# Performance work log

Measured on AMD Instinct MI355X. Metric: run time of the kernel, lower is better.

The kernel has to match this reference:

```python
import jax, jax.numpy as jnp
import numpy as np

DIM = 768
NUM_BLOCKS = 4
BLOCK = DIM // NUM_BLOCKS
SCALE = 0.02


def setup_inputs() -> dict:
    key = jax.random.key(0)
    ks = jax.random.split(key, 7)
    x = jax.random.normal(ks[0], (8, 64, 64, DIM), dtype=jnp.float32)
    w1 = SCALE * jax.random.normal(ks[1], (2, NUM_BLOCKS, BLOCK, BLOCK), dtype=jnp.float32)
    b1 = SCALE * jax.random.normal(ks[2], (2, NUM_BLOCKS, BLOCK), dtype=jnp.float32)
    w2 = SCALE * jax.random.normal(ks[3], (2, NUM_BLOCKS, BLOCK, BLOCK), dtype=jnp.float32)
    b2 = SCALE * jax.random.normal(ks[4], (2, NUM_BLOCKS, BLOCK), dtype=jnp.float32)
    # nn.Linear(dim, dim) weight/bias (kaiming-uniform-ish init; exact init irrelevant for correctness)
    lim = 1.0 / np.sqrt(DIM)
    bias_w = jax.random.uniform(ks[5], (DIM, DIM), minval=-lim, maxval=lim, dtype=jnp.float32)
    bias_b = jax.random.uniform(ks[6], (DIM,), minval=-lim, maxval=lim, dtype=jnp.float32)
    return {"x": x, "w1": w1, "b1": b1, "w2": w2, "b2": b2, "bias_w": bias_w, "bias_b": bias_b}


def _block_mul(t, w):
    # t: (..., nb, bs), w: (nb, bs, bs) -> (..., nb, bs)
    return jnp.einsum('...bd,bdk->...bk', t, w)


def reference(x, w1, b1, w2, b2, bias_w, bias_b):
    B, H, W, C = x.shape
    nb = w1.shape[1]
    bs = C // nb
    bias = x @ bias_w.T + bias_b  # nn.Linear on original x
    xb = x.reshape(B, H, W, nb, bs)
    xf = jnp.fft.rfftn(xb, axes=(1, 2), norm='ortho')  # (B, H, W//2+1, nb, bs) complex
    xr, xi = xf.real, xf.imag
    # layer 1: complex block matmul + bias + relu (relu applied per real/imag part as in source)
    r1 = jax.nn.relu(_block_mul(xr, w1[0]) - _block_mul(xi, w1[1]) + b1[0])
    i1 = jax.nn.relu(_block_mul(xr, w1[1]) + _block_mul(xi, w1[0]) + b1[1])
    # layer 2: NOTE the original torch code reassigns x_real first and then uses the NEW
    # x_real when computing x_imag — we faithfully reproduce that.
    r2 = _block_mul(r1, w2[0]) - _block_mul(i1, w2[1]) + b2[0]
    i2 = _block_mul(r2, w2[1]) + _block_mul(i1, w2[0]) + b2[1]
    xc = jax.lax.complex(r2, i2)
    out = jnp.fft.irfftn(xc, s=(H, W), axes=(1, 2), norm='ortho')
    out = out.reshape(B, H, W, C)
    return out + bias
```

## Files before the change

kernel.cpp:

```cpp
#include <hip/hip_runtime.h>

#define DIM 768
#define NBLK 4
#define BS 192
#define BATCH 8
#define HH 64
#define WW 64
#define KH 33
#define NPTS (BATCH*HH*KH)
#define TWOPI_OVER_64 0.0981747704246810387f
#define LROW 200
#define WSZ (NBLK*BS*BS)

typedef __attribute__((ext_vector_type(8))) short short8;
typedef __attribute__((ext_vector_type(4))) short short4v;
typedef __attribute__((ext_vector_type(4))) float floatx4;
typedef __attribute__((ext_vector_type(4))) unsigned int uint4v;

static __device__ __forceinline__ short f2bs(float f) {
  union { float f; unsigned int i; } v; v.f = f;
  unsigned int x = v.i;
  return (short)((x + 0x7fffu + ((x >> 16) & 1u)) >> 16);
}
static __device__ __forceinline__ float bs2f(short s) {
  union { unsigned int i; float f; } v; v.i = ((unsigned int)(unsigned short)s) << 16; return v.f;
}

#define GLD16(gp, lp) \
  __builtin_amdgcn_global_load_lds( \
      (const __attribute__((address_space(1))) unsigned int*)(gp), \
      (__attribute__((address_space(3))) unsigned int*)(lp), 16, 0, 0)

__global__ __launch_bounds__(256) void k_convx(
    const float* __restrict__ X, short* __restrict__ Xb)
{
  const int i = blockIdx.x * 256 + threadIdx.x;
  const float4* X4 = (const float4*)X;
  #pragma unroll
  for (int it = 0; it < 12; ++it) {
    const int idx = i + it * (2048 * 256);
    const float4 v = X4[idx];
    short4v p = { f2bs(v.x), f2bs(v.y), f2bs(v.z), f2bs(v.w) };
    *(short4v*)&Xb[(size_t)idx * 4] = p;
  }
}

__global__ __launch_bounds__(256) void k_convw(
    const float* __restrict__ W, short* __restrict__ Wb)
{
  const int idx = blockIdx.x * 256 + threadIdx.x;
  const float4 v = ((const float4*)W)[idx];
  short4v p = { f2bs(v.x), f2bs(v.y), f2bs(v.z), f2bs(v.w) };
  *(short4v*)&Wb[(size_t)idx * 4] = p;
}

__global__ __launch_bounds__(256) void k_bias_gemm3(
    const short* __restrict__ Xb, const short* __restrict__ Wb,
    const float* __restrict__ bb, short* __restrict__ Bias)
{
  __shared__ short As[128 * 32];
  __shared__ short Bs[128 * 32];
  const int t = threadIdx.x;
  const int wave = t >> 6, lane = t & 63;
  const int qm = lane & 15, quad = lane >> 4;
  const int wr = (wave >> 1) * 64;
  const int wc = (wave & 1) * 64;
  const int m0 = blockIdx.x * 128, n0 = blockIdx.y * 128;

  floatx4 acc[4][4];
  const floatx4 zero = {0.f, 0.f, 0.f, 0.f};
  #pragma unroll
  for (int ms = 0; ms < 4; ++ms)
    #pragma unroll
    for (int ns = 0; ns < 4; ++ns) acc[ms][ns] = zero;

  const int r0 = t >> 2,        kq0 = (t & 3) * 8;
  const int r1 = (t + 256) >> 2;
  const short* gA0 = &Xb[(size_t)(m0 + r0) * DIM + kq0];
  const short* gA1 = &Xb[(size_t)(m0 + r1) * DIM + kq0];
  const short* gB0 = &Wb[(size_t)(n0 + r0) * DIM + kq0];
  const short* gB1 = &Wb[(size_t)(n0 + r1) * DIM + kq0];
  short* lA0 = &As[wave * 512];
  short* lA1 = &As[wave * 512 + 2048];
  short* lB0 = &Bs[wave * 512];
  short* lB1 = &Bs[wave * 512 + 2048];

  #pragma unroll 1
  for (int k0 = 0; k0 < DIM; k0 += 32) {
    __syncthreads();
    GLD16(gA0 + k0, lA0);
    GLD16(gA1 + k0, lA1);
    GLD16(gB0 + k0, lB0);
    GLD16(gB1 + k0, lB1);
    __syncthreads();

    short8 af[4], bf[4];
    #pragma unroll
    for (int ms = 0; ms < 4; ++ms)
      af[ms] = *(const short8*)&As[(wr + ms*16 + qm) * 32 + quad * 8];
    #pragma unroll
    for (int ns = 0; ns < 4; ++ns)
      bf[ns] = *(const short8*)&Bs[(wc + ns*16 + qm) * 32 + quad * 8];
    #pragma unroll
    for (int ms = 0; ms < 4; ++ms)
      #pragma unroll
      for (int ns = 0; ns < 4; ++ns)
        acc[ms][ns] = __builtin_amdgcn_mfma_f32_16x16x32_bf16(af[ms], bf[ns], acc[ms][ns], 0, 0, 0);
  }

  #pragma unroll
  for (int ns = 0; ns < 4; ++ns) {
    const int col = n0 + wc + ns*16 + qm;
    const float bias = bb[col];
    #pragma unroll
    for (int ms = 0; ms < 4; ++ms)
      #pragma unroll
      for (int r = 0; r < 4; ++r) {
        const int row = m0 + wr + ms*16 + quad*4 + r;
        Bias[(size_t)row * DIM + col] = f2bs(acc[ms][ns][r] + bias);
      }
  }
}

__global__ __launch_bounds__(256) void k_rfft_w_mfma(
    const short* __restrict__ Xb,
    short* __restrict__ Sr, short* __restrict__ Si)
{
  __shared__ short Lx[96 * 72];
  const int t = threadIdx.x;
  const int wave = t >> 6, lane = t & 63;
  const int qm = lane & 15, quad = lane >> 4;
  const int bh = blockIdx.x;
  const int c0 = blockIdx.y * 96;
  const size_t xbase = (size_t)bh * (WW*DIM);
  const size_t obase = (size_t)bh * (KH*DIM);

  #pragma unroll
  for (int it = 0; it < 3; ++it) {
    const int i = t + it * 256;
    const int hd = i & 31;
    const int c4 = i >> 5;
    const size_t g0 = xbase + (size_t)(2*hd) * DIM + c0 + c4 * 4;
    const short4v ra = *(const short4v*)&Xb[g0];
    const short4v rb = *(const short4v*)&Xb[g0 + DIM];
    #pragma unroll
    for (int e = 0; e < 4; ++e) {
      const int d = (c4*4 + e) * 36 + hd;
      ((unsigned*)Lx)[d] = (unsigned)(unsigned short)ra[e] |
                           ((unsigned)(unsigned short)rb[e] << 16);
    }
  }

  short8 Trh[2], Trl[2], Tih[2], Til[2];
  const int krow = wave * 16 + qm;
  #pragma unroll
  for (int kk = 0; kk < 2; ++kk) {
    #pragma unroll
    for (int j = 0; j < 8; ++j) {
      const int w = quad * 8 + j + kk * 32;
      const int ph = (krow * w) & 63;
      float s, c;
      sincosf((float)ph * TWOPI_OVER_64, &s, &c);
      const float tr = c, ti = -s;
      const short trh = f2bs(tr);
      const short tih = f2bs(ti);
      Trh[kk][j] = trh;  Trl[kk][j] = f2bs(tr - bs2f(trh));
      Tih[kk][j] = tih;  Til[kk][j] = f2bs(ti - bs2f(tih));
    }
  }
  __syncthreads();

  if (wave < 3) {
    const floatx4 zero = {0.f, 0.f, 0.f, 0.f};
    #pragma unroll 1
    for (int ct = 0; ct < 6; ++ct) {
      floatx4 Cr = zero, Ci = zero;
      #pragma unroll
      for (int kk = 0; kk < 2; ++kk) {
        const int a = (ct*16 + qm) * 72 + kk*32 + quad*8;
        const short8 xv = *(const short8*)&Lx[a];
        Cr = __builtin_amdgcn_mfma_f32_16x16x32_bf16(Trh[kk], xv, Cr, 0,0,0);
        Cr = __builtin_amdgcn_mfma_f32_16x16x32_bf16(Trl[kk], xv, Cr, 0,0,0);
        Ci = __builtin_amdgcn_mfma_f32_16x16x32_bf16(Tih[kk], xv, Ci, 0,0,0);
        Ci = __builtin_amdgcn_mfma_f32_16x16x32_bf16(Til[kk], xv, Ci, 0,0,0);
      }
      #pragma unroll
      for (int r = 0; r < 4; ++r) {
        const int ko = wave*16 + quad*4 + r;
        if (ko < KH) {
          const size_t o = obase + (size_t)ko * DIM + c0 + ct*16 + qm;
          Sr[o] = f2bs(Cr[r]);
          Si[o] = f2bs(Ci[r]);
        }
      }
    }
  }
}

__global__ __launch_bounds__(256) void k_prep_w(
    const float* __restrict__ w1, const float* __restrict__ w2,
    short* __restrict__ Wout)
{
  const int arr = blockIdx.y;
  const int i = blockIdx.x * 256 + threadIdx.x;
  const int nb = i / (BS*BS);
  const int rem = i % (BS*BS);
  const int n = rem / BS;
  const int d = rem % BS;
  const float* src = (arr < 2) ? w1 : w2;
  const int j = arr & 1;
  const float s = (arr == 3) ? -1.f : 1.f;
  const float v = s * src[((size_t)(j*NBLK + nb) * BS + d) * BS + n];
  Wout[(size_t)arr * WSZ + i] = f2bs(v);
}

__global__ __launch_bounds__(256) void k_prep_w2(
    const float* __restrict__ w2, const float* __restrict__ b2,
    short* __restrict__ Wout, float* __restrict__ b2x)
{
  const int i = blockIdx.x * 256 + threadIdx.x;
  const int n = i % BS;
  const int d = (i / BS) % BS;
  const int nb = i / (BS*BS);
  const float* R = w2 + (size_t)nb * BS * BS;
  const float* I = w2 + ((size_t)NBLK + nb) * BS * BS;
  const float* br = b2 + nb * BS;
  float ri = 0.f, ii = 0.f, bx = 0.f;
  #pragma unroll 4
  for (int m = 0; m < BS; ++m) {
    const float win = I[m*BS + n];
    ri += R[d*BS + m] * win;
    ii += I[d*BS + m] * win;
    bx += br[m] * win;
  }
  const size_t o = ((size_t)nb * BS + n) * BS + d;
  Wout[(size_t)4 * WSZ + o] = f2bs(ri);
  Wout[(size_t)5 * WSZ + o] = f2bs(R[d*BS + n] - ii);
  if (d == 0) b2x[nb * BS + n] = b2[(NBLK + nb) * BS + n] + bx;
}

__global__ __launch_bounds__(256) void k_fmix(
    short* __restrict__ Sr, short* __restrict__ Si,
    const short* __restrict__ WT,
    const float* __restrict__ b1, const float* __restrict__ b2,
    const float* __restrict__ b2x)
{
  __shared__ short U[2 * 64 * LROW];
  short* Ldr = U;
  short* Ldi = U + 192 * 64;
  short* Amr = U;
  short* Ami = U + 64 * LROW;

  const int t = threadIdx.x;
  const int wave = t >> 6, lane = t & 63;
  const int qm = lane & 15, quad = lane >> 4;
  const int bk = blockIdx.x;
  const int b = bk / KH, k = bk % KH;
  const int nb = blockIdx.y;
  const int c0 = nb * BS;
  const size_t hstride = (size_t)KH * DIM;
  const size_t base = ((size_t)b * HH * KH + k) * DIM;

  short8 Ch[2], Cl[2], Sh[2], Sl[2], SNh[2], SNl[2];
  const int hp = wave * 16 + qm;
  #pragma unroll
  for (int kk = 0; kk < 2; ++kk)
    #pragma unroll
    for (int j = 0; j < 8; ++j) {
      const int h = quad*8 + j + kk*32;
      const int ph = (hp * h) & 63;
      float s, c;
      sincosf((float)ph * TWOPI_OVER_64, &s, &c);
      const short ch = f2bs(c), sh = f2bs(s);
      Ch[kk][j] = ch;  Cl[kk][j] = f2bs(c - bs2f(ch));
      Sh[kk][j] = sh;  Sl[kk][j] = f2bs(s - bs2f(sh));
      SNh[kk][j] = (short)(sh ^ (short)0x8000);
      SNl[kk][j] = (short)(Sl[kk][j] ^ (short)0x8000);
    }

  #pragma unroll
  for (int it = 0; it < 6; ++it) {
    const int i = t + it * 256;
    const int hd = i & 31;
    const int c4 = i >> 5;
    const size_t g0 = base + (size_t)(2*hd) * hstride + c0 + c4 * 4;
    const short4v ra = *(const short4v*)&Sr[g0];
    const short4v rb = *(const short4v*)&Sr[g0 + hstride];
    const short4v ia = *(const short4v*)&Si[g0];
    const short4v ib = *(const short4v*)&Si[g0 + hstride];
    #pragma unroll
    for (int e = 0; e < 4; ++e) {
      const int c = c4*4 + e;
      const int d = c * 32 + (hd ^ ((c & 7) << 2));
      ((unsigned*)Ldr)[d] = (unsigned)(unsigned short)ra[e] |
                            ((unsigned)(unsigned short)rb[e] << 16);
      ((unsigned*)Ldi)[d] = (unsigned)(unsigned short)ia[e] |
                            ((unsigned)(unsigned short)ib[e] << 16);
    }
  }
  __syncthreads();

  const floatx4 zero = {0.f, 0.f, 0.f, 0.f};
  floatx4 Fr[12], Fi[12];
  #pragma unroll
  for (int ct = 0; ct < 12; ++ct) { Fr[ct] = zero; Fi[ct] = zero; }
  #pragma unroll
  for (int ct = 0; ct < 12; ++ct)
    #pragma unroll
    for (int kk = 0; kk < 2; ++kk) {
      const int a = (ct*16 + qm) * 64 + ((kk*32 + quad*8) ^ ((qm & 7) << 3));
      const short8 sr = *(const short8*)&Ldr[a];
      const short8 si = *(const short8*)&Ldi[a];
      Fr[ct] = __builtin_amdgcn_mfma_f32_16x16x32_bf16(Ch[kk],  sr, Fr[ct], 0,0,0);
      Fr[ct] = __builtin_amdgcn_mfma_f32_16x16x32_bf16(Cl[kk],  sr, Fr[ct], 0,0,0);
      Fr[ct] = __builtin_amdgcn_mfma_f32_16x16x32_bf16(Sh[kk],  si, Fr[ct], 0,0,0);
      Fr[ct] = __builtin_amdgcn_mfma_f32_16x16x32_bf16(Sl[kk],  si, Fr[ct], 0,0,0);
      Fi[ct] = __builtin_amdgcn_mfma_f32_16x16x32_bf16(SNh[kk], sr, Fi[ct], 0,0,0);
      Fi[ct] = __builtin_amdgcn_mfma_f32_16x16x32_bf16(SNl[kk], sr, Fi[ct], 0,0,0);
      Fi[ct] = __builtin_amdgcn_mfma_f32_16x16x32_bf16(Ch[kk],  si, Fi[ct], 0,0,0);
      Fi[ct] = __builtin_amdgcn_mfma_f32_16x16x32_bf16(Cl[kk],  si, Fi[ct], 0,0,0);
    }
  __syncthreads();

  #pragma unroll
  for (int ct = 0; ct < 12; ++ct)
    #pragma unroll
    for (int r = 0; r < 4; ++r) {
      const int row = wave*16 + quad*4 + r;
      const int c = ct*16 + qm;
      Amr[row * LROW + c] = f2bs(Fr[ct][r] * 0.015625f);
      Ami[row * LROW + c] = f2bs(Fi[ct][r] * 0.015625f);
    }
  __syncthreads();

  const short* W1R  = WT;
  const short* W1I  = WT + 1 * (size_t)WSZ;
  const short* W2R  = WT + 2 * (size_t)WSZ;
  const short* W2IN = WT + 3 * (size_t)WSZ;
  const short* W2RI = WT + 4 * (size_t)WSZ;
  const short* W2X  = WT + 5 * (size_t)WSZ;

  int nl[3];
  size_t wb[3];
  #pragma unroll
  for (int nt = 0; nt < 3; ++nt) {
    nl[nt] = wave * 48 + nt * 16 + qm;
    wb[nt] = (size_t)(c0 + nl[nt]) * BS + quad * 8;
  }

  floatx4 aR[4][3], aI[4][3];
  #pragma unroll
  for (int ms = 0; ms < 4; ++ms)
    #pragma unroll
    for (int nt = 0; nt < 3; ++nt) { aR[ms][nt] = zero; aI[ms][nt] = zero; }

  #pragma unroll 1
  for (int k0 = 0; k0 < BS; k0 += 32) {
    short8 xr[4], xi[4];
    #pragma unroll
    for (int ms = 0; ms < 4; ++ms) {
      const int a = (ms*16 + qm) * LROW + k0 + quad * 8;
      xr[ms] = *(const short8*)&Amr[a];
      xi[ms] = *(const short8*)&Ami[a];
    }
    #pragma unroll
    for (int nt = 0; nt < 3; ++nt) {
      const short8 br = *(const short8*)&W1R[wb[nt] + k0];
      const short8 bi = *(const short8*)&W1I[wb[nt] + k0];
      short8 bin;
      *(uint4v*)&bin = *(const uint4v*)&bi ^ 0x80008000u;
      #pragma unroll
      for (int ms = 0; ms < 4; ++ms) {
        aR[ms][nt] = __builtin_amdgcn_mfma_f32_16x16x32_bf16(xr[ms], br,  aR[ms][nt], 0,0,0);
        aR[ms][nt] = __builtin_amdgcn_mfma_f32_16x16x32_bf16(xi[ms], bin, aR[ms][nt], 0,0,0);
        aI[ms][nt] = __builtin_amdgcn_mfma_f32_16x16x32_bf16(xr[ms], bi,  aI[ms][nt], 0,0,0);
        aI[ms][nt] = __builtin_amdgcn_mfma_f32_16x16x32_bf16(xi[ms], br,  aI[ms][nt], 0,0,0);
      }
    }
  }
  __syncthreads();
  #pragma unroll
  for (int nt = 0; nt < 3; ++nt) {
    const float b1r = b1[nb * BS + nl[nt]];
    const float b1i = b1[(NBLK + nb) * BS + nl[nt]];
    #pragma unroll
    for (int ms = 0; ms < 4; ++ms)
      #pragma unroll
      for (int r = 0; r < 4; ++r) {
        const int row = ms*16 + quad*4 + r;
        Amr[row * LROW + nl[nt]] = f2bs(fmaxf(aR[ms][nt][r] + b1r, 0.f));
        Ami[row * LROW + nl[nt]] = f2bs(fmaxf(aI[ms][nt][r] + b1i, 0.f));
      }
  }
  __syncthreads();

  floatx4 c2r[4][3], c2i[4][3];
  #pragma unroll
  for (int ms = 0; ms < 4; ++ms)
    #pragma unroll
    for (int nt = 0; nt < 3; ++nt) { c2r[ms][nt] = zero; c2i[ms][nt] = zero; }

  #pragma unroll 1
  for (int k0 = 0; k0 < BS; k0 += 32) {
    short8 r1[4], i1[4];
    #pragma unroll
    for (int ms = 0; ms < 4; ++ms) {
      const int a = (ms*16 + qm) * LROW + k0 + quad * 8;
      r1[ms] = *(const short8*)&Amr[a];
      i1[ms] = *(const short8*)&Ami[a];
    }
    #pragma unroll
    for (int nt = 0; nt < 3; ++nt) {
      const short8 w_r  = *(const short8*)&W2R [wb[nt] + k0];
      const short8 w_in = *(const short8*)&W2IN[wb[nt] + k0];
      const short8 w_ri = *(const short8*)&W2RI[wb[nt] + k0];
      const short8 w_x  = *(const short8*)&W2X [wb[nt] + k0];
      #pragma unroll
      for (int ms = 0; ms < 4; ++ms) {
        c2r[ms][nt] = __builtin_amdgcn_mfma_f32_16x16x32_bf16(r1[ms], w_r,  c2r[ms][nt], 0,0,0);
        c2r[ms][nt] = __builtin_amdgcn_mfma_f32_16x16x32_bf16(i1[ms], w_in, c2r[ms][nt], 0,0,0);
        c2i[ms][nt] = __builtin_amdgcn_mfma_f32_16x16x32_bf16(r1[ms], w_ri, c2i[ms][nt], 0,0,0);
        c2i[ms][nt] = __builtin_amdgcn_mfma_f32_16x16x32_bf16(i1[ms], w_x,  c2i[ms][nt], 0,0,0);
      }
    }
  }
  __syncthreads();

  #pragma unroll
  for (int nt = 0; nt < 3; ++nt) {
    const float b2r = b2 [nb * BS + nl[nt]];
    const float bxi = b2x[nb * BS + nl[nt]];
    const int c = nl[nt];
    #pragma unroll
    for (int ms = 0; ms < 4; ++ms)
      #pragma unroll
      for (int r = 0; r < 4; ++r) {
        const int row = ms*16 + quad*4 + r;
        const int d = c * 64 + (row ^ ((c & 7) << 3));
        Ldr[d] = f2bs(c2r[ms][nt][r] + b2r);
        Ldi[d] = f2bs(c2i[ms][nt][r] + bxi);
      }
  }
  __syncthreads();

  #pragma unroll 1
  for (int ct = 0; ct < 12; ++ct) {
    floatx4 Cr = zero, Ci = zero;
    #pragma unroll
    for (int kk = 0; kk < 2; ++kk) {
      const int a = (ct*16 + qm) * 64 + ((kk*32 + quad*8) ^ ((qm & 7) << 3));
      const short8 gr = *(const short8*)&Ldr[a];
      const short8 gi = *(const short8*)&Ldi[a];
      Cr = __builtin_amdgcn_mfma_f32_16x16x32_bf16(Ch[kk],  gr, Cr, 0,0,0);
      Cr = __builtin_amdgcn_mfma_f32_16x16x32_bf16(Cl[kk],  gr, Cr, 0,0,0);
      Cr = __builtin_amdgcn_mfma_f32_16x16x32_bf16(SNh[kk], gi, Cr, 0,0,0);
      Cr = __builtin_amdgcn_mfma_f32_16x16x32_bf16(SNl[kk], gi, Cr, 0,0,0);
      Ci = __builtin_amdgcn_mfma_f32_16x16x32_bf16(Sh[kk],  gr, Ci, 0,0,0);
      Ci = __builtin_amdgcn_mfma_f32_16x16x32_bf16(Sl[kk],  gr, Ci, 0,0,0);
      Ci = __builtin_amdgcn_mfma_f32_16x16x32_bf16(Ch[kk],  gi, Ci, 0,0,0);
      Ci = __builtin_amdgcn_mfma_f32_16x16x32_bf16(Cl[kk],  gi, Ci, 0,0,0);
    }
    #pragma unroll
    for (int r = 0; r < 4; ++r) {
      const int hpo = wave*16 + quad*4 + r;
      const size_t o = base + (size_t)hpo * hstride + c0 + ct*16 + qm;
      Sr[o] = f2bs(Cr[r]);
      Si[o] = f2bs(Ci[r]);
    }
  }
}

__global__ __launch_bounds__(256) void k_irfft_w_mfma(
    const short* __restrict__ Sr, const short* __restrict__ Si,
    const short* __restrict__ Bias, float* __restrict__ out)
{
  __shared__ short Lr[96 * 72];
  __shared__ short Li[96 * 72];
  const int t = threadIdx.x;
  const int wave = t >> 6, lane = t & 63;
  const int qm = lane & 15, quad = lane >> 4;
  const int bh = blockIdx.x;
  const int c0 = blockIdx.y * 96;
  const size_t gbase = (size_t)bh * (KH*DIM);
  const size_t obase = (size_t)bh * (WW*DIM);

  #pragma unroll
  for (int it = 0; it < 3; ++it) {
    const int i = t + it * 256;
    const int hd = i & 31;
    const int c4 = i >> 5;
    const int ka = 2*hd, kb = 2*hd + 1;
    short4v ra = {0,0,0,0}, rb = ra, ia = ra, ib = ra;
    if (ka < KH) {
      const size_t g0 = gbase + (size_t)ka * DIM + c0 + c4 * 4;
      ra = *(const short4v*)&Sr[g0];
      ia = *(const short4v*)&Si[g0];
    }
    if (kb < KH) {
      const size_t g1 = gbase + (size_t)kb * DIM + c0 + c4 * 4;
      rb = *(const short4v*)&Sr[g1];
      ib = *(const short4v*)&Si[g1];
    }
    #pragma unroll
    for (int e = 0; e < 4; ++e) {
      const int d = (c4*4 + e) * 36 + hd;
      ((unsigned*)Lr)[d] = (unsigned)(unsigned short)ra[e] |
                           ((unsigned)(unsigned short)rb[e] << 16);
      ((unsigned*)Li)[d] = (unsigned)(unsigned short)ia[e] |
                           ((unsigned)(unsigned short)ib[e] << 16);
    }
  }

  short8 Arh[2], Arl[2], Aih[2], Ail[2];
  const int wrow = wave * 16 + qm;
  #pragma unroll
  for (int kk = 0; kk < 2; ++kk) {
    #pragma unroll
    for (int j = 0; j < 8; ++j) {
      const int k = quad * 8 + j + kk * 32;
      float ar = 0.f, ai = 0.f;
      if (k < KH) {
        const int ph = (wrow * k) & 63;
        float s, c;
        sincosf((float)ph * TWOPI_OVER_64, &s, &c);
        const float ck = (k == 0 || k == 32) ? (1.0f/64.0f) : (2.0f/64.0f);
        ar = ck * c;
        ai = -ck * s;
      }
      const short arh = f2bs(ar);
      const short aih = f2bs(ai);
      Arh[kk][j] = arh;  Arl[kk][j] = f2bs(ar - bs2f(arh));
      Aih[kk][j] = aih;  Ail[kk][j] = f2bs(ai - bs2f(aih));
    }
  }
  __syncthreads();

  const floatx4 zero = {0.f, 0.f, 0.f, 0.f};
  #pragma unroll 1
  for (int ct = 0; ct < 6; ++ct) {
    floatx4 C = zero;
    #pragma unroll
    for (int kk = 0; kk < 2; ++kk) {
      const int a = (ct*16 + qm) * 72 + kk*32 + quad*8;
      const short8 gr = *(const short8*)&Lr[a];
      const short8 gi = *(const short8*)&Li[a];
      C = __builtin_amdgcn_mfma_f32_16x16x32_bf16(Arh[kk], gr, C, 0,0,0);
      C = __builtin_amdgcn_mfma_f32_16x16x32_bf16(Arl[kk], gr, C, 0,0,0);
      C = __builtin_amdgcn_mfma_f32_16x16x32_bf16(Aih[kk], gi, C, 0,0,0);
      C = __builtin_amdgcn_mfma_f32_16x16x32_bf16(Ail[kk], gi, C, 0,0,0);
    }
    #pragma unroll
    for (int r = 0; r < 4; ++r) {
      const int w = wave*16 + quad*4 + r;
      const size_t o = obase + (size_t)w * DIM + c0 + ct*16 + qm;
      out[o] = C[r] + bs2f(Bias[o]);
    }
  }
}

extern "C" void kernel_launch(void* const* d_in, const int* in_sizes, int n_in,
                              void* d_out, int out_size, void* d_ws, size_t ws_size,
                              hipStream_t stream) {
  const float* x  = (const float*)d_in[0];
  const float* w1 = (const float*)d_in[1];
  const float* b1 = (const float*)d_in[2];
  const float* w2 = (const float*)d_in[3];
  const float* b2 = (const float*)d_in[4];
  const float* bw = (const float*)d_in[5];
  const float* bb = (const float*)d_in[6];
  float* out = (float*)d_out;

  short* Sr = (short*)d_ws;
  short* Si = Sr + (size_t)NPTS * DIM;
  short* WT = Si + (size_t)NPTS * DIM;
  short* Xb = WT + (size_t)6 * WSZ;
  short* Wb = Xb + (size_t)BATCH * HH * WW * DIM;
  short* Bias = Wb + (size_t)DIM * DIM;
  float* b2x = (float*)(Bias + (size_t)BATCH * HH * WW * DIM);

  k_convx<<<2048, 256, 0, stream>>>(x, Xb);
  k_convw<<<(DIM*DIM/4)/256, 256, 0, stream>>>(bw, Wb);
  k_prep_w<<<dim3(WSZ/256, 4), 256, 0, stream>>>(w1, w2, WT);
  k_prep_w2<<<dim3(WSZ/256), 256, 0, stream>>>(w2, b2, WT, b2x);
  k_bias_gemm3<<<dim3(32768/128, DIM/128), 256, 0, stream>>>(Xb, Wb, bb, Bias);
  k_rfft_w_mfma<<<dim3(BATCH*HH, DIM/96), 256, 0, stream>>>(Xb, Sr, Si);
  k_fmix<<<dim3(BATCH*KH, NBLK), 256, 0, stream>>>(Sr, Si, WT, b1, b2, b2x);
  k_irfft_w_mfma<<<dim3(BATCH*HH, DIM/96), 256, 0, stream>>>(Sr, Si, Bias, out);
}
```

Before: 493.5 us.

## Issue global loads early to overlap with twiddle setup and prefetch weights

In the rfft, irfft and fmix kernels, global loads are hoisted into registers before the sincos twiddle generation, so memory latency overlaps with trig computation; the LDS stores happen afterwards. fmix switches to 16-byte loads and a padded LDS layout (stride 72) instead of the XOR swizzle. It also software-prefetches the next W1 k-slice during layer-1 MFMAs and batches the W2 loads ahead of their MFMA loop. Register pressure and LDS footprint grow, which may reduce occupancy, and the padded layout may change bank-conflict behaviour.

```diff
diff --git a/kernel.cpp b/kernel.cpp
--- a/kernel.cpp
+++ b/kernel.cpp
@@ -135,20 +135,15 @@
   const size_t xbase = (size_t)bh * (WW*DIM);
   const size_t obase = (size_t)bh * (KH*DIM);
 
+  const int hd = t & 31;
+  const int c4b = t >> 5;
+  short4v ra[3], rb[3];
   #pragma unroll
   for (int it = 0; it < 3; ++it) {
-    const int i = t + it * 256;
-    const int hd = i & 31;
-    const int c4 = i >> 5;
+    const int c4 = c4b + it * 8;
     const size_t g0 = xbase + (size_t)(2*hd) * DIM + c0 + c4 * 4;
-    const short4v ra = *(const short4v*)&Xb[g0];
-    const short4v rb = *(const short4v*)&Xb[g0 + DIM];
-    #pragma unroll
-    for (int e = 0; e < 4; ++e) {
-      const int d = (c4*4 + e) * 36 + hd;
-      ((unsigned*)Lx)[d] = (unsigned)(unsigned short)ra[e] |
-                           ((unsigned)(unsigned short)rb[e] << 16);
-    }
+    ra[it] = *(const short4v*)&Xb[g0];
+    rb[it] = *(const short4v*)&Xb[g0 + DIM];
   }
 
   short8 Trh[2], Trl[2], Tih[2], Til[2];
@@ -166,6 +161,17 @@
       const short tih = f2bs(ti);
       Trh[kk][j] = trh;  Trl[kk][j] = f2bs(tr - bs2f(trh));
       Tih[kk][j] = tih;  Til[kk][j] = f2bs(ti - bs2f(tih));
+    }
+  }
+
+  #pragma unroll
+  for (int it = 0; it < 3; ++it) {
+    const int c4 = c4b + it * 8;
+    #pragma unroll
+    for (int e = 0; e < 4; ++e) {
+      const int d = (c4*4 + e) * 36 + hd;
+      ((unsigned*)Lx)[d] = (unsigned)(unsigned short)ra[it][e] |
+                           ((unsigned)(unsigned short)rb[it][e] << 16);
     }
   }
   __syncthreads();
@@ -245,9 +251,9 @@
     const float* __restrict__ b1, const float* __restrict__ b2,
     const float* __restrict__ b2x)
 {
-  __shared__ short U[2 * 64 * LROW];
+  __shared__ short U[2 * 192 * 72];
   short* Ldr = U;
-  short* Ldi = U + 192 * 64;
+  short* Ldi = U + 192 * 72;
   short* Amr = U;
   short* Ami = U + 64 * LROW;
 
@@ -260,6 +266,39 @@
   const int c0 = nb * BS;
   const size_t hstride = (size_t)KH * DIM;
   const size_t base = ((size_t)b * HH * KH + k) * DIM;
+
+  const int hd = t & 31;
+  const int c8b = t >> 5;
+  short8 ra[3], rb[3], ia[3], ib[3];
+  #pragma unroll
+  for (int it = 0; it < 3; ++it) {
+    const int c8 = c8b + it * 8;
+    const size_t g0 = base + (size_t)(2*hd) * hstride + c0 + c8 * 8;
+    ra[it] = *(const short8*)&Sr[g0];
+    rb[it] = *(const short8*)&Sr[g0 + hstride];
+    ia[it] = *(const short8*)&Si[g0];
+    ib[it] = *(const short8*)&Si[g0 + hstride];
+  }
+
+  const short* W1R  = WT;
+  const short* W1I  = WT + 1 * (size_t)WSZ;
+  const short* W2R  = WT + 2 * (size_t)WSZ;
+  const short* W2IN = WT + 3 * (size_t)WSZ;
+  const short* W2RI = WT + 4 * (size_t)WSZ;
+  const short* W2X  = WT + 5 * (size_t)WSZ;
+  int nl[3];
+  size_t wb[3];
+  #pragma unroll
+  for (int nt = 0; nt < 3; ++nt) {
+    nl[nt] = wave * 48 + nt * 16 + qm;
+    wb[nt] = (size_t)(c0 + nl[nt]) * BS + quad * 8;
+  }
+  short8 w1r[3], w1i[3];
+  #pragma unroll
+  for (int nt = 0; nt < 3; ++nt) {
+    w1r[nt] = *(const short8*)&W1R[wb[nt]];
+    w1i[nt] = *(const short8*)&W1I[wb[nt]];
+  }
 
   short8 Ch[2], Cl[2], Sh[2], Sl[2], SNh[2], SNl[2];
   const int hp = wave * 16 + qm;
@@ -279,23 +318,15 @@
     }
 
   #pragma unroll
-  for (int it = 0; it < 6; ++it) {
-    const int i = t + it * 256;
-    const int hd = i & 31;
-    const int c4 = i >> 5;
-    const size_t g0 = base + (size_t)(2*hd) * hstride + c0 + c4 * 4;
-    const short4v ra = *(const short4v*)&Sr[g0];
-    const short4v rb = *(const short4v*)&Sr[g0 + hstride];
-    const short4v ia = *(const short4v*)&Si[g0];
-    const short4v ib = *(const short4v*)&Si[g0 + hstride];
-    #pragma unroll
-    for (int e = 0; e < 4; ++e) {
-      const int c = c4*4 + e;
-      const int d = c * 32 + (hd ^ ((c & 7) << 2));
-      ((unsigned*)Ldr)[d] = (unsigned)(unsigned short)ra[e] |
-                            ((unsigned)(unsigned short)rb[e] << 16);
-      ((unsigned*)Ldi)[d] = (unsigned)(unsigned short)ia[e] |
-                            ((unsigned)(unsigned short)ib[e] << 16);
+  for (int it = 0; it < 3; ++it) {
+    const int c8 = c8b + it * 8;
+    #pragma unroll
+    for (int e = 0; e < 8; ++e) {
+      const int d = (c8*8 + e) * 36 + hd;
+      ((unsigned*)Ldr)[d] = (unsigned)(unsigned short)ra[it][e] |
+                            ((unsigned)(unsigned short)rb[it][e] << 16);
+      ((unsigned*)Ldi)[d] = (unsigned)(unsigned short)ia[it][e] |
+                            ((unsigned)(unsigned short)ib[it][e] << 16);
     }
   }
   __syncthreads();
@@ -308,7 +339,7 @@
   for (int ct = 0; ct < 12; ++ct)
     #pragma unroll
     for (int kk = 0; kk < 2; ++kk) {
-      const int a = (ct*16 + qm) * 64 + ((kk*32 + quad*8) ^ ((qm & 7) << 3));
+      const int a = (ct*16 + qm) * 72 + kk*32 + quad*8;
       const short8 sr = *(const short8*)&Ldr[a];
       const short8 si = *(const short8*)&Ldi[a];
       Fr[ct] = __builtin_amdgcn_mfma_f32_16x16x32_bf16(Ch[kk],  sr, Fr[ct], 0,0,0);
@@ -333,21 +364,6 @@
     }
   __syncthreads();
 
-  const short* W1R  = WT;
-  const short* W1I  = WT + 1 * (size_t)WSZ;
-  const short* W2R  = WT + 2 * (size_t)WSZ;
-  const short* W2IN = WT + 3 * (size_t)WSZ;
-  const short* W2RI = WT + 4 * (size_t)WSZ;
-  const short* W2X  = WT + 5 * (size_t)WSZ;
-
-  int nl[3];
-  size_t wb[3];
-  #pragma unroll
-  for (int nt = 0; nt < 3; ++nt) {
-    nl[nt] = wave * 48 + nt * 16 + qm;
-    wb[nt] = (size_t)(c0 + nl[nt]) * BS + quad * 8;
-  }
-
   floatx4 aR[4][3], aI[4][3];
   #pragma unroll
   for (int ms = 0; ms < 4; ++ms)
@@ -363,18 +379,27 @@
       xr[ms] = *(const short8*)&Amr[a];
       xi[ms] = *(const short8*)&Ami[a];
     }
+    short8 cwr[3], cwi[3];
+    #pragma unroll
+    for (int nt = 0; nt < 3; ++nt) { cwr[nt] = w1r[nt]; cwi[nt] = w1i[nt]; }
+    const int kn = k0 + 32;
+    if (kn < BS) {
+      #pragma unroll
+      for (int nt = 0; nt < 3; ++nt) {
+        w1r[nt] = *(const short8*)&W1R[wb[nt] + kn];
+        w1i[nt] = *(const short8*)&W1I[wb[nt] + kn];
+      }
+    }
     #pragma unroll
     for (int nt = 0; nt < 3; ++nt) {
-      const short8 br = *(const short8*)&W1R[wb[nt] + k0];
-      const short8 bi = *(const short8*)&W1I[wb[nt] + k0];
       short8 bin;
-      *(uint4v*)&bin = *(const uint4v*)&bi ^ 0x80008000u;
+      *(uint4v*)&bin = *(const uint4v*)&cwi[nt] ^ 0x80008000u;
       #pragma unroll
       for (int ms = 0; ms < 4; ++ms) {
-        aR[ms][nt] = __builtin_amdgcn_mfma_f32_16x16x32_bf16(xr[ms], br,  aR[ms][nt], 0,0,0);
-        aR[ms][nt] = __builtin_amdgcn_mfma_f32_16x16x32_bf16(xi[ms], bin, aR[ms][nt], 0,0,0);
-        aI[ms][nt] = __builtin_amdgcn_mfma_f32_16x16x32_bf16(xr[ms], bi,  aI[ms][nt], 0,0,0);
-        aI[ms][nt] = __builtin_amdgcn_mfma_f32_16x16x32_bf16(xi[ms], br,  aI[ms][nt], 0,0,0);
+        aR[ms][nt] = __builtin_amdgcn_mfma_f32_16x16x32_bf16(xr[ms], cwr[nt], aR[ms][nt], 0,0,0);
+        aR[ms][nt] = __builtin_amdgcn_mfma_f32_16x16x32_bf16(xi[ms], bin,     aR[ms][nt], 0,0,0);
+        aI[ms][nt] = __builtin_amdgcn_mfma_f32_16x16x32_bf16(xr[ms], cwi[nt], aI[ms][nt], 0,0,0);
+        aI[ms][nt] = __builtin_amdgcn_mfma_f32_16x16x32_bf16(xi[ms], cwr[nt], aI[ms][nt], 0,0,0);
       }
     }
   }
@@ -409,18 +434,22 @@
       r1[ms] = *(const short8*)&Amr[a];
       i1[ms] = *(const short8*)&Ami[a];
     }
+    short8 w_r[3], w_in[3], w_ri[3], w_x[3];
     #pragma unroll
     for (int nt = 0; nt < 3; ++nt) {
-      const short8 w_r  = *(const short8*)&W2R [wb[nt] + k0];
-      const short8 w_in = *(const short8*)&W2IN[wb[nt] + k0];
-      const short8 w_ri = *(const short8*)&W2RI[wb[nt] + k0];
-      const short8 w_x  = *(const short8*)&W2X [wb[nt] + k0];
+      w_r [nt] = *(const short8*)&W2R [wb[nt] + k0];
+      w_in[nt] = *(const short8*)&W2IN[wb[nt] + k0];
+      w_ri[nt] = *(const short8*)&W2RI[wb[nt] + k0];
+      w_x [nt] = *(const short8*)&W2X [wb[nt] + k0];
+    }
+    #pragma unroll
+    for (int nt = 0; nt < 3; ++nt) {
       #pragma unroll
       for (int ms = 0; ms < 4; ++ms) {
-        c2r[ms][nt] = __builtin_amdgcn_mfma_f32_16x16x32_bf16(r1[ms], w_r,  c2r[ms][nt], 0,0,0);
-        c2r[ms][nt] = __builtin_amdgcn_mfma_f32_16x16x32_bf16(i1[ms], w_in, c2r[ms][nt], 0,0,0);
-        c2i[ms][nt] = __builtin_amdgcn_mfma_f32_16x16x32_bf16(r1[ms], w_ri, c2i[ms][nt], 0,0,0);
-        c2i[ms][nt] = __builtin_amdgcn_mfma_f32_16x16x32_bf16(i1[ms], w_x,  c2i[ms][nt], 0,0,0);
+        c2r[ms][nt] = __builtin_amdgcn_mfma_f32_16x16x32_bf16(r1[ms], w_r [nt], c2r[ms][nt], 0,0,0);
+        c2r[ms][nt] = __builtin_amdgcn_mfma_f32_16x16x32_bf16(i1[ms], w_in[nt], c2r[ms][nt], 0,0,0);
+        c2i[ms][nt] = __builtin_amdgcn_mfma_f32_16x16x32_bf16(r1[ms], w_ri[nt], c2i[ms][nt], 0,0,0);
+        c2i[ms][nt] = __builtin_amdgcn_mfma_f32_16x16x32_bf16(i1[ms], w_x [nt], c2i[ms][nt], 0,0,0);
       }
     }
   }
@@ -436,9 +465,8 @@
       #pragma unroll
       for (int r = 0; r < 4; ++r) {
         const int row = ms*16 + quad*4 + r;
-        const int d = c * 64 + (row ^ ((c & 7) << 3));
-        Ldr[d] = f2bs(c2r[ms][nt][r] + b2r);
-        Ldi[d] = f2bs(c2i[ms][nt][r] + bxi);
+        Ldr[c * 72 + row] = f2bs(c2r[ms][nt][r] + b2r);
+        Ldi[c * 72 + row] = f2bs(c2i[ms][nt][r] + bxi);
       }
   }
   __syncthreads();
@@ -448,7 +476,7 @@
     floatx4 Cr = zero, Ci = zero;
     #pragma unroll
     for (int kk = 0; kk < 2; ++kk) {
-      const int a = (ct*16 + qm) * 64 + ((kk*32 + quad*8) ^ ((qm & 7) << 3));
+      const int a = (ct*16 + qm) * 72 + kk*32 + quad*8;
       const short8 gr = *(const short8*)&Ldr[a];
       const short8 gi = *(const short8*)&Ldi[a];
       Cr = __builtin_amdgcn_mfma_f32_16x16x32_bf16(Ch[kk],  gr, Cr, 0,0,0);
@@ -484,30 +512,24 @@
   const size_t gbase = (size_t)bh * (KH*DIM);
   const size_t obase = (size_t)bh * (WW*DIM);
 
+  const int hd = t & 31;
+  const int c4b = t >> 5;
+  short4v ra[3], rb[3], ia[3], ib[3];
   #pragma unroll
   for (int it = 0; it < 3; ++it) {
-    const int i = t + it * 256;
-    const int hd = i & 31;
-    const int c4 = i >> 5;
+    const int c4 = c4b + it * 8;
     const int ka = 2*hd, kb = 2*hd + 1;
-    short4v ra = {0,0,0,0}, rb = ra, ia = ra, ib = ra;
+    short4v z = {0,0,0,0};
+    ra[it] = z; rb[it] = z; ia[it] = z; ib[it] = z;
     if (ka < KH) {
       const size_t g0 = gbase + (size_t)ka * DIM + c0 + c4 * 4;
-      ra = *(const short4v*)&Sr[g0];
-      ia = *(const short4v*)&Si[g0];
+      ra[it] = *(const short4v*)&Sr[g0];
+      ia[it] = *(const short4v*)&Si[g0];
     }
     if (kb < KH) {
       const size_t g1 = gbase + (size_t)kb * DIM + c0 + c4 * 4;
-      rb = *(const short4v*)&Sr[g1];
-      ib = *(const short4v*)&Si[g1];
-    }
-    #pragma unroll
-    for (int e = 0; e < 4; ++e) {
-      const int d = (c4*4 + e) * 36 + hd;
-      ((unsigned*)Lr)[d] = (unsigned)(unsigned short)ra[e] |
-                           ((unsigned)(unsigned short)rb[e] << 16);
-      ((unsigned*)Li)[d] = (unsigned)(unsigned short)ia[e] |
-                           ((unsigned)(unsigned short)ib[e] << 16);
+      rb[it] = *(const short4v*)&Sr[g1];
+      ib[it] = *(const short4v*)&Si[g1];
     }
   }
 
@@ -531,6 +553,19 @@
       const short aih = f2bs(ai);
       Arh[kk][j] = arh;  Arl[kk][j] = f2bs(ar - bs2f(arh));
       Aih[kk][j] = aih;  Ail[kk][j] = f2bs(ai - bs2f(aih));
+    }
+  }
+
+  #pragma unroll
+  for (int it = 0; it < 3; ++it) {
+    const int c4 = c4b + it * 8;
+    #pragma unroll
+    for (int e = 0; e < 4; ++e) {
+      const int d = (c4*4 + e) * 36 + hd;
+      ((unsigned*)Lr)[d] = (unsigned)(unsigned short)ra[it][e] |
+                           ((unsigned)(unsigned short)rb[it][e] << 16);
+      ((unsigned*)Li)[d] = (unsigned)(unsigned short)ia[it][e] |
+                           ((unsigned)(unsigned short)ib[it][e] << 16);
     }
   }
   __syncthreads();
```

New measurement: 481.9 us. 1.02x faster.
